# Kernel tuning notes

Measured on AMD Instinct MI355X. Metric: run time of the kernel, lower is better.

## Reference

```python
import jax, jax.numpy as jnp
import numpy as np

N_NODES = 50000
N_EDGES = 800000
D_FEAT = 96
HIDDEN = 256
OUT = 40


def setup_inputs() -> dict:
    key = jax.random.key(0)
    ks = jax.random.split(key, 10)
    features = jax.random.normal(ks[0], (N_NODES, D_FEAT), dtype=jnp.float32)
    src = jax.random.randint(ks[1], (N_EDGES,), 0, N_NODES, dtype=jnp.int32)
    dst = jax.random.randint(ks[2], (N_EDGES,), 0, N_NODES, dtype=jnp.int32)
    def lin(k, fan_in, fan_out):
        bound = 1.0 / np.sqrt(fan_in)
        kw, kb = jax.random.split(k)
        W = jax.random.uniform(kw, (fan_in, fan_out), jnp.float32, -bound, bound)
        b = jax.random.uniform(kb, (fan_out,), jnp.float32, -bound, bound)
        return W, b
    W1, b1 = lin(ks[3], 2 * D_FEAT, HIDDEN)
    W2, b2 = lin(ks[4], HIDDEN, HIDDEN)
    W3, b3 = lin(ks[5], HIDDEN, OUT)
    return {"features": features, "src": src, "dst": dst,
            "W1": W1, "b1": b1, "W2": W2, "b2": b2, "W3": W3, "b3": b3}


def reference(features, src, dst, W1, b1, W2, b2, W3, b3):
    # neighbor mean: gather src features, segment-sum into dst, divide by degree
    gathered = features[src]                                  # [E, D]
    summed = jax.ops.segment_sum(gathered, dst, num_segments=N_NODES)  # [N, D]
    deg = jax.ops.segment_sum(jnp.ones((N_EDGES,), jnp.float32), dst,
                              num_segments=N_NODES)           # [N]
    neighbor_feats = summed / jnp.maximum(deg, 1.0)[:, None]  # zero where no neighbors
    combined = jnp.concatenate([features, neighbor_feats], axis=1)  # [N, 2D]
    x = jax.nn.relu(combined @ W1 + b1)
    x = jax.nn.relu(x @ W2 + b2)
    return x @ W3 + b3
```

## Files before the change

### kernel.cpp

```cpp
#include <hip/hip_runtime.h>

#define N_NODES 50000
#define N_EDGES 800000
#define DF      96
#define HID     256
#define OUTF    40
#define BM      64
#define NPART   256
#define PCAP    4096

#define EPB     2048
#define NBE     ((N_EDGES + EPB - 1) / EPB)
#define CS      48

#define FEAT_THREADS (N_NODES * DF / 8)
#define FEAT_BLKS ((FEAT_THREADS + 255) / 256)
#define WSHUF_ELEMS ((96 + 128 + 24) * 512)
#define WSHUF_BLKS (WSHUF_ELEMS / 256)

typedef __attribute__((ext_vector_type(8))) short bf16x8;
typedef __attribute__((ext_vector_type(4))) float f32x4;

static __device__ __forceinline__ unsigned short f2bf(float f) {
    unsigned int u = __float_as_uint(f);
    u += 0x7fffu + ((u >> 16) & 1u);
    return (unsigned short)(u >> 16);
}
static __device__ __forceinline__ int part_of(int d) { return (d * NPART) / N_NODES; }
static __device__ __forceinline__ int part_n0(int p) { return (p * N_NODES + NPART - 1) >> 8; }

__global__ __launch_bounds__(256) void k1_prep_bin(
    const float* __restrict__ feat, const float* __restrict__ W1,
    const float* __restrict__ W2, const float* __restrict__ W3,
    const int* __restrict__ src, const int* __restrict__ dst,
    uint4* __restrict__ featbf, unsigned short* __restrict__ W1s,
    unsigned short* __restrict__ W2s, unsigned short* __restrict__ W3s,
    unsigned int* __restrict__ packed2, int* __restrict__ cellCnt)
{
    const int bid = blockIdx.x, t = threadIdx.x;
    if (bid < FEAT_BLKS) {
        int i = bid * 256 + t;
        if (i < FEAT_THREADS) {
            const float4* p = reinterpret_cast<const float4*>(feat) + (size_t)i * 2;
            float4 v0 = p[0], v1 = p[1];
            uint4 pk;
            pk.x = (unsigned)f2bf(v0.x) | ((unsigned)f2bf(v0.y) << 16);
            pk.y = (unsigned)f2bf(v0.z) | ((unsigned)f2bf(v0.w) << 16);
            pk.z = (unsigned)f2bf(v1.x) | ((unsigned)f2bf(v1.y) << 16);
            pk.w = (unsigned)f2bf(v1.z) | ((unsigned)f2bf(v1.w) << 16);
            featbf[i] = pk;
        }
        return;
    }
    if (bid < FEAT_BLKS + WSHUF_BLKS) {
        int i = (bid - FEAT_BLKS) * 256 + t;
        int j  = i & 7;
        int l  = (i >> 3) & 63;
        int fi = i >> 9;
        int kg = l >> 4, n16 = l & 15;
        if (fi < 96) {
            int tt = fi / 6, s = fi % 6;
            int k = s * 32 + kg * 8 + j, n = tt * 16 + n16;
            W1s[i] = f2bf(W1[(size_t)k * HID + n]);
        } else if (fi < 96 + 128) {
            int f2 = fi - 96;
            int tt = f2 / 8, s = f2 % 8;
            int k = s * 32 + kg * 8 + j, n = tt * 16 + n16;
            W2s[i - 96 * 512] = f2bf(W2[(size_t)k * HID + n]);
        } else {
            int f3 = fi - 224;
            int tt = f3 / 8, s = f3 % 8;
            int k = s * 32 + kg * 8 + j, n = tt * 16 + n16;
            W3s[i - 224 * 512] = (n < OUTF) ? f2bf(W3[(size_t)k * OUTF + n])
                                            : (unsigned short)0;
        }
        return;
    }
    {
        __shared__ int cur[NPART];
        const int bid2 = bid - FEAT_BLKS - WSHUF_BLKS;
        cur[t] = 0;
        __syncthreads();
        int pv[8], pos[8];
        unsigned pkv[8];
        bool valid[8];
#pragma unroll
        for (int k = 0; k < 8; ++k) {
            int e = bid2 * EPB + k * 256 + t;
            valid[k] = (e < N_EDGES);
            pv[k] = 0; pkv[k] = 0; pos[k] = CS;
            if (valid[k]) {
                int d = dst[e], s = src[e];
                int p = part_of(d);
                pv[k] = p;
                pkv[k] = ((unsigned)(d - part_n0(p)) << 16) | (unsigned)s;
                pos[k] = atomicAdd(&cur[p], 1);
            }
        }
        __syncthreads();
        cellCnt[t * NBE + bid2] = (cur[t] < CS) ? cur[t] : CS;
#pragma unroll
        for (int k = 0; k < 8; ++k) {
            if (valid[k] && pos[k] < CS)
                packed2[((size_t)pv[k] * NBE + bid2) * CS + pos[k]] = pkv[k];
        }
    }
}

__global__ __launch_bounds__(256) void partB(
    const unsigned int* __restrict__ packed2, const int* __restrict__ cellCnt,
    int* __restrict__ counts, int* __restrict__ offs,
    unsigned short* __restrict__ sorted16)
{
    __shared__ int hist[NPART];
    __shared__ int scanex[NPART];
    __shared__ int cur[NPART];
    __shared__ int totalSh;
    __shared__ unsigned short srcLDS[PCAP];
    const int p = blockIdx.x, t = threadIdx.x;
    const int n0 = part_n0(p), n1 = part_n0(p + 1);
    const int nl = n1 - n0;
    const unsigned int* cells = packed2 + (size_t)p * NBE * CS;
    const int* ccnt = cellCnt + (size_t)p * NBE;

    hist[t] = 0;
    __syncthreads();
    for (int c = t; c < NBE; c += 256) {
        int cnt = ccnt[c];
        const unsigned int* cp = cells + (size_t)c * CS;
        for (int i = 0; i < cnt; ++i)
            atomicAdd(&hist[cp[i] >> 16], 1);
    }
    __syncthreads();
    int v = hist[t];
    scanex[t] = v;
    __syncthreads();
    for (int off = 1; off < NPART; off <<= 1) {
        int x = (t >= off) ? scanex[t - off] : 0;
        __syncthreads();
        scanex[t] += x;
        __syncthreads();
    }
    int ex = scanex[t] - v;
    cur[t] = ex;
    if (t < nl) {
        counts[n0 + t] = v;
        offs[n0 + t] = p * PCAP + ex;
    }
    if (t == NPART - 1) totalSh = scanex[NPART - 1];
    __syncthreads();
    for (int c = t; c < NBE; c += 256) {
        int cnt = ccnt[c];
        const unsigned int* cp = cells + (size_t)c * CS;
        for (int i = 0; i < cnt; ++i) {
            unsigned pk = cp[i];
            int r = atomicAdd(&cur[pk >> 16], 1);
            srcLDS[r] = (unsigned short)(pk & 0xffffu);
        }
    }
    __syncthreads();
    const int total = totalSh;
    for (int i = t; i < total; i += 256)
        sorted16[p * PCAP + i] = srcLDS[i];
}

__global__ __launch_bounds__(256) void aggregate(
    const unsigned int* __restrict__ featbf,
    const unsigned short* __restrict__ sorted16,
    const int* __restrict__ offs, const int* __restrict__ counts,
    unsigned int* __restrict__ nbr32)
{
    int gw = (blockIdx.x * 256 + threadIdx.x) >> 6;
    int lane = threadIdx.x & 63;
    if (gw >= N_NODES) return;
    int beg = offs[gw];
    int cnt = counts[gw];
    const unsigned short* sp = sorted16 + beg;
    const bool act = (lane < 48);
    float a0 = 0.f, a1 = 0.f;
    int j = 0;
    for (; j + 8 <= cnt; j += 8) {
        unsigned u[8];
        if (act) {
#pragma unroll
            for (int q = 0; q < 8; ++q)
                u[q] = featbf[(size_t)sp[j + q] * 48 + lane];
#pragma unroll
            for (int q = 0; q < 8; ++q) {
                a0 += __uint_as_float(u[q] << 16);
                a1 += __uint_as_float(u[q] & 0xffff0000u);
            }
        }
    }
    for (; j + 2 <= cnt; j += 2) {
        if (act) {
            unsigned u0 = featbf[(size_t)sp[j] * 48 + lane];
            unsigned u1 = featbf[(size_t)sp[j + 1] * 48 + lane];
            a0 += __uint_as_float(u0 << 16) + __uint_as_float(u1 << 16);
            a1 += __uint_as_float(u0 & 0xffff0000u) + __uint_as_float(u1 & 0xffff0000u);
        }
    }
    if (j < cnt && act) {
        unsigned u0 = featbf[(size_t)sp[j] * 48 + lane];
        a0 += __uint_as_float(u0 << 16);
        a1 += __uint_as_float(u0 & 0xffff0000u);
    }
    float inv = 1.0f / fmaxf((float)cnt, 1.0f);
    if (act)
        nbr32[(size_t)gw * 48 + lane] =
            (unsigned)f2bf(a0 * inv) | ((unsigned)f2bf(a1 * inv) << 16);
}

__global__ __launch_bounds__(512, 4) void mlp3(
    const unsigned int* __restrict__ featbf, const unsigned int* __restrict__ nbr32,
    const unsigned short* __restrict__ W1s, const float* __restrict__ b1,
    const unsigned short* __restrict__ W2s, const float* __restrict__ b2,
    const unsigned short* __restrict__ W3s, const float* __restrict__ b3,
    float* __restrict__ out)
{
    __shared__ __align__(16) char bufA[BM * 512];
    __shared__ __align__(16) char bufB[BM * 512];

    const int t = threadIdx.x;
    const int lane = t & 63;
    const int w = t >> 6;
    const int row0 = blockIdx.x * BM;
    const int n16 = lane & 15;
    const int kg = lane >> 4;

    for (int i = t; i < BM * 24; i += 512) {
        int row = i / 24, c = i % 24;
        int half = (c >= 12) ? 1 : 0;
        int cg = c - half * 12;
        int grow = row0 + row;
        int lds_byte = (row * 384 + half * 192 + cg * 16) ^ ((row & 7) << 4);
        uint4 v = make_uint4(0u, 0u, 0u, 0u);
        if (grow < N_NODES) {
            const unsigned int* s = half ? nbr32 : featbf;
            v = *reinterpret_cast<const uint4*>(s + (size_t)grow * 48 + cg * 4);
        }
        *reinterpret_cast<uint4*>(bufA + lds_byte) = v;
    }
    __syncthreads();

    {
        f32x4 acc[4][2];
#pragma unroll
        for (int tt = 0; tt < 2; ++tt) {
            float bb = b1[(w * 2 + tt) * 16 + n16];
#pragma unroll
            for (int mt = 0; mt < 4; ++mt) {
                acc[mt][tt][0] = bb; acc[mt][tt][1] = bb;
                acc[mt][tt][2] = bb; acc[mt][tt][3] = bb;
            }
        }
#pragma unroll
        for (int s = 0; s < 6; ++s) {
            bf16x8 a[4], b[2];
#pragma unroll
            for (int mt = 0; mt < 4; ++mt) {
                int m = mt * 16 + n16;
                int byte_ = (m * 384 + s * 64 + kg * 16) ^ ((m & 7) << 4);
                a[mt] = *reinterpret_cast<const bf16x8*>(bufA + byte_);
            }
#pragma unroll
            for (int tt = 0; tt < 2; ++tt)
                b[tt] = *reinterpret_cast<const bf16x8*>(
                    W1s + ((size_t)((w * 2 + tt) * 6 + s) * 64 + lane) * 8);
#pragma unroll
            for (int mt = 0; mt < 4; ++mt)
#pragma unroll
                for (int tt = 0; tt < 2; ++tt)
                    acc[mt][tt] = __builtin_amdgcn_mfma_f32_16x16x32_bf16(
                        a[mt], b[tt], acc[mt][tt], 0, 0, 0);
        }
#pragma unroll
        for (int mt = 0; mt < 4; ++mt)
#pragma unroll
            for (int tt = 0; tt < 2; ++tt) {
                int col = (w * 2 + tt) * 16 + n16;
#pragma unroll
                for (int r = 0; r < 4; ++r) {
                    int row = mt * 16 + kg * 4 + r;
                    int byte_ = (row * 512 + col * 2) ^ ((row & 7) << 4);
                    *reinterpret_cast<unsigned short*>(bufB + byte_) =
                        f2bf(fmaxf(acc[mt][tt][r], 0.f));
                }
            }
    }
    __syncthreads();

    {
        f32x4 acc[4][2];
#pragma unroll
        for (int tt = 0; tt < 2; ++tt) {
            float bb = b2[(w * 2 + tt) * 16 + n16];
#pragma unroll
            for (int mt = 0; mt < 4; ++mt) {
                acc[mt][tt][0] = bb; acc[mt][tt][1] = bb;
                acc[mt][tt][2] = bb; acc[mt][tt][3] = bb;
            }
        }
#pragma unroll
        for (int s = 0; s < 8; ++s) {
            bf16x8 a[4], b[2];
#pragma unroll
            for (int mt = 0; mt < 4; ++mt) {
                int m = mt * 16 + n16;
                int byte_ = (m * 512 + s * 64 + kg * 16) ^ ((m & 7) << 4);
                a[mt] = *reinterpret_cast<const bf16x8*>(bufB + byte_);
            }
#pragma unroll
            for (int tt = 0; tt < 2; ++tt)
                b[tt] = *reinterpret_cast<const bf16x8*>(
                    W2s + ((size_t)((w * 2 + tt) * 8 + s) * 64 + lane) * 8);
#pragma unroll
            for (int mt = 0; mt < 4; ++mt)
#pragma unroll
                for (int tt = 0; tt < 2; ++tt)
                    acc[mt][tt] = __builtin_amdgcn_mfma_f32_16x16x32_bf16(
                        a[mt], b[tt], acc[mt][tt], 0, 0, 0);
        }
#pragma unroll
        for (int mt = 0; mt < 4; ++mt)
#pragma unroll
            for (int tt = 0; tt < 2; ++tt) {
                int col = (w * 2 + tt) * 16 + n16;
#pragma unroll
                for (int r = 0; r < 4; ++r) {
                    int row = mt * 16 + kg * 4 + r;
                    int byte_ = (row * 512 + col * 2) ^ ((row & 7) << 4);
                    *reinterpret_cast<unsigned short*>(bufA + byte_) =
                        f2bf(fmaxf(acc[mt][tt][r], 0.f));
                }
            }
    }
    __syncthreads();

    {
        const int mt3 = w & 3;
        const int tb  = (w >> 2) ? 2 : 0;
        const int nt3 = (w >> 2) ? 1 : 2;
        f32x4 acc3[2];
#pragma unroll
        for (int tt = 0; tt < 2; ++tt) {
            int col = (tb + tt) * 16 + n16;
            float bb = (tt < nt3 && col < OUTF) ? b3[col] : 0.f;
            acc3[tt][0] = bb; acc3[tt][1] = bb; acc3[tt][2] = bb; acc3[tt][3] = bb;
        }
#pragma unroll
        for (int s = 0; s < 8; ++s) {
            int m = mt3 * 16 + n16;
            int byte_ = (m * 512 + s * 64 + kg * 16) ^ ((m & 7) << 4);
            bf16x8 a = *reinterpret_cast<const bf16x8*>(bufA + byte_);
#pragma unroll
            for (int tt = 0; tt < 2; ++tt) {
                if (tt < nt3) {
                    bf16x8 b = *reinterpret_cast<const bf16x8*>(
                        W3s + ((size_t)((tb + tt) * 8 + s) * 64 + lane) * 8);
                    acc3[tt] = __builtin_amdgcn_mfma_f32_16x16x32_bf16(
                        a, b, acc3[tt], 0, 0, 0);
                }
            }
        }
#pragma unroll
        for (int tt = 0; tt < 2; ++tt) {
            int col = (tb + tt) * 16 + n16;
            if (tt < nt3 && col < OUTF) {
#pragma unroll
                for (int r = 0; r < 4; ++r) {
                    int row = row0 + mt3 * 16 + kg * 4 + r;
                    if (row < N_NODES)
                        out[(size_t)row * OUTF + col] = acc3[tt][r];
                }
            }
        }
    }
}

extern "C" void kernel_launch(void* const* d_in, const int* in_sizes, int n_in,
                              void* d_out, int out_size, void* d_ws, size_t ws_size,
                              hipStream_t stream)
{
    const float* feat = (const float*)d_in[0];
    const int*   src  = (const int*)d_in[1];
    const int*   dst  = (const int*)d_in[2];
    const float* W1   = (const float*)d_in[3];
    const float* b1   = (const float*)d_in[4];
    const float* W2   = (const float*)d_in[5];
    const float* b2   = (const float*)d_in[6];
    const float* W3   = (const float*)d_in[7];
    const float* b3   = (const float*)d_in[8];
    float* out = (float*)d_out;

    int* cellCnt = (int*)d_ws;
    int* counts  = cellCnt + NPART * NBE;
    int* offs    = counts + N_NODES;
    unsigned int* packed2 = (unsigned int*)(offs + N_NODES);
    unsigned short* sorted16 = (unsigned short*)(packed2 + (size_t)NPART * NBE * CS);
    unsigned int* featbf = (unsigned int*)(sorted16 + NPART * PCAP);
    unsigned int* nbr32  = featbf + (size_t)N_NODES * 48;
    unsigned short* W1s  = (unsigned short*)(nbr32 + (size_t)N_NODES * 48);
    unsigned short* W2s  = W1s + 96 * 512;
    unsigned short* W3s  = W2s + 128 * 512;

    k1_prep_bin<<<FEAT_BLKS + WSHUF_BLKS + NBE, 256, 0, stream>>>(
        feat, W1, W2, W3, src, dst,
        (uint4*)featbf, W1s, W2s, W3s, packed2, cellCnt);

    partB<<<NPART, 256, 0, stream>>>(packed2, cellCnt, counts, offs, sorted16);

    aggregate<<<(N_NODES * 64 + 255) / 256, 256, 0, stream>>>(
        featbf, sorted16, offs, counts, nbr32);

    mlp3<<<(N_NODES + BM - 1) / BM, 512, 0, stream>>>(
        featbf, nbr32, W1s, b1, W2s, b2, W3s, b3, out);
}
```

Measured before the change: 84.66 us.

## Fuse partition sort and neighbor aggregation into one kernel with finer partitions

```diff
diff --git a/kernel.cpp b/kernel.cpp
--- a/kernel.cpp
+++ b/kernel.cpp
@@ -6,12 +6,12 @@
 #define HID     256
 #define OUTF    40
 #define BM      64
-#define NPART   256
-#define PCAP    4096
+#define NPART   512
+#define CS      32
+#define PCAP2   2048
 
 #define EPB     2048
 #define NBE     ((N_EDGES + EPB - 1) / EPB)
-#define CS      48
 
 #define FEAT_THREADS (N_NODES * DF / 8)
 #define FEAT_BLKS ((FEAT_THREADS + 255) / 256)
@@ -26,8 +26,12 @@
     u += 0x7fffu + ((u >> 16) & 1u);
     return (unsigned short)(u >> 16);
 }
-static __device__ __forceinline__ int part_of(int d) { return (d * NPART) / N_NODES; }
-static __device__ __forceinline__ int part_n0(int p) { return (p * N_NODES + NPART - 1) >> 8; }
+static __device__ __forceinline__ int part_of(int d) {
+    return (int)(((long long)d * NPART) / N_NODES);
+}
+static __device__ __forceinline__ int part_n0(int p) {
+    return (int)(((long long)p * N_NODES + NPART - 1) / NPART);
+}
 
 __global__ __launch_bounds__(256) void k1_prep_bin(
     const float* __restrict__ feat, const float* __restrict__ W1,
@@ -80,6 +84,7 @@
         __shared__ int cur[NPART];
         const int bid2 = bid - FEAT_BLKS - WSHUF_BLKS;
         cur[t] = 0;
+        cur[t + 256] = 0;
         __syncthreads();
         int pv[8], pos[8];
         unsigned pkv[8];
@@ -98,7 +103,11 @@
             }
         }
         __syncthreads();
-        cellCnt[t * NBE + bid2] = (cur[t] < CS) ? cur[t] : CS;
+#pragma unroll
+        for (int q = 0; q < 2; ++q) {
+            int pp = q * 256 + t;
+            cellCnt[(size_t)pp * NBE + bid2] = (cur[pp] < CS) ? cur[pp] : CS;
+        }
 #pragma unroll
         for (int k = 0; k < 8; ++k) {
             if (valid[k] && pos[k] < CS)
@@ -107,108 +116,97 @@
     }
 }
 
-__global__ __launch_bounds__(256) void partB(
+__global__ __launch_bounds__(1024, 4) void part_agg(
     const unsigned int* __restrict__ packed2, const int* __restrict__ cellCnt,
-    int* __restrict__ counts, int* __restrict__ offs,
-    unsigned short* __restrict__ sorted16)
+    const unsigned int* __restrict__ featbf, unsigned int* __restrict__ nbr32)
 {
-    __shared__ int hist[NPART];
-    __shared__ int scanex[NPART];
-    __shared__ int cur[NPART];
-    __shared__ int totalSh;
-    __shared__ unsigned short srcLDS[PCAP];
+    __shared__ int hist[128];
+    __shared__ int scanex[128];
+    __shared__ int cur[128];
+    __shared__ int nodeOff[128];
+    __shared__ int nodeCnt[128];
+    __shared__ unsigned short srcLDS[PCAP2];
     const int p = blockIdx.x, t = threadIdx.x;
-    const int n0 = part_n0(p), n1 = part_n0(p + 1);
-    const int nl = n1 - n0;
+    const int n0 = part_n0(p);
+    const int nl = part_n0(p + 1) - n0;
     const unsigned int* cells = packed2 + (size_t)p * NBE * CS;
     const int* ccnt = cellCnt + (size_t)p * NBE;
 
-    hist[t] = 0;
-    __syncthreads();
-    for (int c = t; c < NBE; c += 256) {
+    if (t < 128) hist[t] = 0;
+    __syncthreads();
+    for (int c = t; c < NBE; c += 1024) {
         int cnt = ccnt[c];
         const unsigned int* cp = cells + (size_t)c * CS;
         for (int i = 0; i < cnt; ++i)
             atomicAdd(&hist[cp[i] >> 16], 1);
     }
     __syncthreads();
-    int v = hist[t];
-    scanex[t] = v;
-    __syncthreads();
-    for (int off = 1; off < NPART; off <<= 1) {
-        int x = (t >= off) ? scanex[t - off] : 0;
+    int v = 0;
+    if (t < 128) { v = hist[t]; scanex[t] = v; }
+    __syncthreads();
+    for (int off = 1; off < 128; off <<= 1) {
+        int x = 0;
+        if (t < 128 && t >= off) x = scanex[t - off];
         __syncthreads();
-        scanex[t] += x;
+        if (t < 128) scanex[t] += x;
         __syncthreads();
     }
-    int ex = scanex[t] - v;
-    cur[t] = ex;
-    if (t < nl) {
-        counts[n0 + t] = v;
-        offs[n0 + t] = p * PCAP + ex;
-    }
-    if (t == NPART - 1) totalSh = scanex[NPART - 1];
-    __syncthreads();
-    for (int c = t; c < NBE; c += 256) {
+    if (t < 128) {
+        int ex = scanex[t] - v;
+        cur[t] = ex;
+        nodeOff[t] = ex;
+        nodeCnt[t] = v;
+    }
+    __syncthreads();
+    for (int c = t; c < NBE; c += 1024) {
         int cnt = ccnt[c];
         const unsigned int* cp = cells + (size_t)c * CS;
         for (int i = 0; i < cnt; ++i) {
             unsigned pk = cp[i];
             int r = atomicAdd(&cur[pk >> 16], 1);
-            srcLDS[r] = (unsigned short)(pk & 0xffffu);
-        }
-    }
-    __syncthreads();
-    const int total = totalSh;
-    for (int i = t; i < total; i += 256)
-        sorted16[p * PCAP + i] = srcLDS[i];
-}
-
-__global__ __launch_bounds__(256) void aggregate(
-    const unsigned int* __restrict__ featbf,
-    const unsigned short* __restrict__ sorted16,
-    const int* __restrict__ offs, const int* __restrict__ counts,
-    unsigned int* __restrict__ nbr32)
-{
-    int gw = (blockIdx.x * 256 + threadIdx.x) >> 6;
-    int lane = threadIdx.x & 63;
-    if (gw >= N_NODES) return;
-    int beg = offs[gw];
-    int cnt = counts[gw];
-    const unsigned short* sp = sorted16 + beg;
+            if (r < PCAP2) srcLDS[r] = (unsigned short)(pk & 0xffffu);
+        }
+    }
+    __syncthreads();
+    const int wv = t >> 6, lane = t & 63;
     const bool act = (lane < 48);
-    float a0 = 0.f, a1 = 0.f;
-    int j = 0;
-    for (; j + 8 <= cnt; j += 8) {
-        unsigned u[8];
-        if (act) {
-#pragma unroll
-            for (int q = 0; q < 8; ++q)
-                u[q] = featbf[(size_t)sp[j + q] * 48 + lane];
-#pragma unroll
-            for (int q = 0; q < 8; ++q) {
-                a0 += __uint_as_float(u[q] << 16);
-                a1 += __uint_as_float(u[q] & 0xffff0000u);
-            }
-        }
-    }
-    for (; j + 2 <= cnt; j += 2) {
-        if (act) {
-            unsigned u0 = featbf[(size_t)sp[j] * 48 + lane];
-            unsigned u1 = featbf[(size_t)sp[j + 1] * 48 + lane];
-            a0 += __uint_as_float(u0 << 16) + __uint_as_float(u1 << 16);
-            a1 += __uint_as_float(u0 & 0xffff0000u) + __uint_as_float(u1 & 0xffff0000u);
-        }
-    }
-    if (j < cnt && act) {
-        unsigned u0 = featbf[(size_t)sp[j] * 48 + lane];
-        a0 += __uint_as_float(u0 << 16);
-        a1 += __uint_as_float(u0 & 0xffff0000u);
-    }
-    float inv = 1.0f / fmaxf((float)cnt, 1.0f);
-    if (act)
-        nbr32[(size_t)gw * 48 + lane] =
-            (unsigned)f2bf(a0 * inv) | ((unsigned)f2bf(a1 * inv) << 16);
+    for (int n = wv; n < nl; n += 16) {
+        int beg = nodeOff[n];
+        int cnt = nodeCnt[n];
+        float a0 = 0.f, a1 = 0.f;
+        int j = 0;
+        for (; j + 8 <= cnt; j += 8) {
+            unsigned u[8];
+            if (act) {
+#pragma unroll
+                for (int q = 0; q < 8; ++q)
+                    u[q] = featbf[(size_t)srcLDS[beg + j + q] * 48 + lane];
+#pragma unroll
+                for (int q = 0; q < 8; ++q) {
+                    a0 += __uint_as_float(u[q] << 16);
+                    a1 += __uint_as_float(u[q] & 0xffff0000u);
+                }
+            }
+        }
+        for (; j + 2 <= cnt; j += 2) {
+            if (act) {
+                unsigned u0 = featbf[(size_t)srcLDS[beg + j] * 48 + lane];
+                unsigned u1 = featbf[(size_t)srcLDS[beg + j + 1] * 48 + lane];
+                a0 += __uint_as_float(u0 << 16) + __uint_as_float(u1 << 16);
+                a1 += __uint_as_float(u0 & 0xffff0000u)
+                    + __uint_as_float(u1 & 0xffff0000u);
+            }
+        }
+        if (j < cnt && act) {
+            unsigned u0 = featbf[(size_t)srcLDS[beg + j] * 48 + lane];
+            a0 += __uint_as_float(u0 << 16);
+            a1 += __uint_as_float(u0 & 0xffff0000u);
+        }
+        float inv = 1.0f / fmaxf((float)cnt, 1.0f);
+        if (act)
+            nbr32[(size_t)(n0 + n) * 48 + lane] =
+                (unsigned)f2bf(a0 * inv) | ((unsigned)f2bf(a1 * inv) << 16);
+    }
 }
 
 __global__ __launch_bounds__(512, 4) void mlp3(
@@ -394,11 +392,8 @@
     float* out = (float*)d_out;
 
     int* cellCnt = (int*)d_ws;
-    int* counts  = cellCnt + NPART * NBE;
-    int* offs    = counts + N_NODES;
-    unsigned int* packed2 = (unsigned int*)(offs + N_NODES);
-    unsigned short* sorted16 = (unsigned short*)(packed2 + (size_t)NPART * NBE * CS);
-    unsigned int* featbf = (unsigned int*)(sorted16 + NPART * PCAP);
+    unsigned int* packed2 = (unsigned int*)(cellCnt + (size_t)NPART * NBE);
+    unsigned int* featbf = packed2 + (size_t)NPART * NBE * CS;
     unsigned int* nbr32  = featbf + (size_t)N_NODES * 48;
     unsigned short* W1s  = (unsigned short*)(nbr32 + (size_t)N_NODES * 48);
     unsigned short* W2s  = W1s + 96 * 512;
@@ -408,10 +403,7 @@
         feat, W1, W2, W3, src, dst,
         (uint4*)featbf, W1s, W2s, W3s, packed2, cellCnt);
 
-    partB<<<NPART, 256, 0, stream>>>(packed2, cellCnt, counts, offs, sorted16);
-
-    aggregate<<<(N_NODES * 64 + 255) / 256, 256, 0, stream>>>(
-        featbf, sorted16, offs, counts, nbr32);
+    part_agg<<<NPART, 1024, 0, stream>>>(packed2, cellCnt, featbf, nbr32);
 
     mlp3<<<(N_NODES + BM - 1) / BM, 512, 0, stream>>>(
         featbf, nbr32, W1s, b1, W2s, b2, W3s, b3, out);
```

After: 79.01 us (median of 3 runs). 6.7% less time.
